# Kernel tuning notes

Measured on AMD Instinct MI355X. Metric: run time of the kernel, lower is better.

The kernel has to match this reference:

```python
import jax, jax.numpy as jnp
import numpy as np

B, M, N = 2097152, 6, 3
SQUARINGS = 8   # fixed scaling: ||T||_F <~ sqrt(M) ~ 2.5, so ||A|| ~ 0.01 after scaling
ORDER = 12     # Taylor order; gives ~machine precision at this scaled norm


def _expm(T):
    """Batched matrix exponential via fixed scaling-and-squaring + Horner Taylor.
    T: [B, N, N]. Numerically matches torch.matrix_exp for these well-scaled inputs."""
    A = T / (2.0 ** SQUARINGS)
    I = jnp.eye(T.shape[-1], dtype=T.dtype)
    # Horner: exp(A) ~ I + A(I + A/2(I + ... (I + A/ORDER)))
    E = I + A / ORDER
    for k in range(ORDER - 1, 0, -1):
        E = I + jnp.matmul(A / k, E)
    for _ in range(SQUARINGS):
        E = jnp.matmul(E, E)
    return E


def setup_inputs() -> dict:
    key = jax.random.key(0)
    kx, kc, kp = jax.random.split(key, 3)
    x = jax.random.normal(kx, (B, N, 1), dtype=jnp.float32)
    c = jax.random.normal(kc, (B, M), dtype=jnp.float32)
    psi = jax.random.normal(kp, (M, N, N), dtype=jnp.float32) * 0.1
    # per-dictionary-element Frobenius normalization, as in __init__
    psi = psi / jnp.linalg.norm(psi.reshape(M, -1), axis=1)[:, None, None]
    return {"x": x, "c": c, "psi": psi}


def reference(x, c, psi):
    # T[b] = sum_m c[b,m] * psi[m]  -> [B, N, N]
    T = jnp.einsum('bm,mij->bij', c, psi)
    return jnp.matmul(_expm(T), x)  # [B, N, 1]
```

## Files before the change

kernel.cpp:

```cpp
#include <hip/hip_runtime.h>

__global__ __launch_bounds__(256) void expm_kernel(
    const float* __restrict__ x,
    const float* __restrict__ c,
    const float* __restrict__ psi,
    float* __restrict__ out,
    int B)
{
    const int b = blockIdx.x * blockDim.x + threadIdx.x;
    if (b >= B) return;

    const float2* c2 = reinterpret_cast<const float2*>(c + (size_t)b * 6);
    const float2 ca = c2[0], cb = c2[1], cc = c2[2];
    const float cm[6] = {ca.x * 0.0625f, ca.y * 0.0625f,
                         cb.x * 0.0625f, cb.y * 0.0625f,
                         cc.x * 0.0625f, cc.y * 0.0625f};

    float A[9];
#pragma unroll
    for (int j = 0; j < 9; ++j) {
        float s = cm[0] * psi[0 * 9 + j];
#pragma unroll
        for (int m = 1; m < 6; ++m) s = fmaf(cm[m], psi[m * 9 + j], s);
        A[j] = s;
    }

    float E[9];
#pragma unroll
    for (int j = 0; j < 9; ++j) E[j] = A[j] * (1.0f / 6.0f);
    E[0] += 1.0f; E[4] += 1.0f; E[8] += 1.0f;

#pragma unroll
    for (int k = 5; k >= 1; --k) {
        const float rk = 1.0f / (float)k;
        float Tm[9];
#pragma unroll
        for (int i = 0; i < 3; ++i) {
#pragma unroll
            for (int j = 0; j < 3; ++j) {
                float s = A[i * 3 + 0] * E[0 * 3 + j];
                s = fmaf(A[i * 3 + 1], E[1 * 3 + j], s);
                s = fmaf(A[i * 3 + 2], E[2 * 3 + j], s);
                Tm[i * 3 + j] = s;
            }
        }
#pragma unroll
        for (int j = 0; j < 9; ++j) E[j] = fmaf(Tm[j], rk, (j == 0 || j == 4 || j == 8) ? 1.0f : 0.0f);
    }

#pragma unroll
    for (int s4 = 0; s4 < 2; ++s4) {
        float Tm[9];
#pragma unroll
        for (int i = 0; i < 3; ++i) {
#pragma unroll
            for (int j = 0; j < 3; ++j) {
                float v = E[i * 3 + 0] * E[0 * 3 + j];
                v = fmaf(E[i * 3 + 1], E[1 * 3 + j], v);
                v = fmaf(E[i * 3 + 2], E[2 * 3 + j], v);
                Tm[i * 3 + j] = v;
            }
        }
#pragma unroll
        for (int j = 0; j < 9; ++j) E[j] = Tm[j];
    }

    const float* xb = x + (size_t)b * 3;
    float y0 = xb[0], y1 = xb[1], y2 = xb[2];
#pragma unroll
    for (int r = 0; r < 4; ++r) {
        const float t0 = fmaf(E[0], y0, fmaf(E[1], y1, E[2] * y2));
        const float t1 = fmaf(E[3], y0, fmaf(E[4], y1, E[5] * y2));
        const float t2 = fmaf(E[6], y0, fmaf(E[7], y1, E[8] * y2));
        y0 = t0; y1 = t1; y2 = t2;
    }

    float* ob = out + (size_t)b * 3;
    ob[0] = y0; ob[1] = y1; ob[2] = y2;
}

extern "C" void kernel_launch(void* const* d_in, const int* in_sizes, int n_in,
                              void* d_out, int out_size, void* d_ws, size_t ws_size,
                              hipStream_t stream) {
    const float* x   = (const float*)d_in[0];
    const float* c   = (const float*)d_in[1];
    const float* psi = (const float*)d_in[2];
    float* out = (float*)d_out;

    const int B = in_sizes[1] / 6;
    const int block = 256;
    const int grid = (B + block - 1) / block;
    expm_kernel<<<grid, block, 0, stream>>>(x, c, psi, out, B);
}
```

Baseline: 108.7 us.

## Replace Taylor Horner chain with Cayley-Hamilton quadratic polynomial for 3x3 expm

Computes the trace, principal-minor sum and determinant of the scaled 3x3 matrix, then runs a scalar recurrence to reduce the order-12 Taylor series to a0*I + a1*A + a2*A^2 via Cayley-Hamilton. This removes five 3x3 matmuls of Horner and two squarings, leaving one A^2 product. The scaling changes from 1/16 to 1/4 with only the final four matrix-vector repetitions left, so accuracy relies on the truncated series at a larger norm and on the numerical stability of the recurrence.

After: 104.8 us. -3.6%, faster.

```diff
diff --git a/kernel.cpp b/kernel.cpp
--- a/kernel.cpp
+++ b/kernel.cpp
@@ -12,9 +12,9 @@
 
     const float2* c2 = reinterpret_cast<const float2*>(c + (size_t)b * 6);
     const float2 ca = c2[0], cb = c2[1], cc = c2[2];
-    const float cm[6] = {ca.x * 0.0625f, ca.y * 0.0625f,
-                         cb.x * 0.0625f, cb.y * 0.0625f,
-                         cc.x * 0.0625f, cc.y * 0.0625f};
+    const float cm[6] = {ca.x * 0.25f, ca.y * 0.25f,
+                         cb.x * 0.25f, cb.y * 0.25f,
+                         cc.x * 0.25f, cc.y * 0.25f};
 
     float A[9];
 #pragma unroll
@@ -25,45 +25,53 @@
         A[j] = s;
     }
 
+    const float tr = A[0] + A[4] + A[8];
+    const float m01 = fmaf(A[0], A[4], -A[1] * A[3]);
+    const float m02 = fmaf(A[0], A[8], -A[2] * A[6]);
+    const float m12 = fmaf(A[4], A[8], -A[5] * A[7]);
+    const float msum = m01 + m02 + m12;
+    const float M10 = fmaf(A[3], A[8], -A[5] * A[6]);
+    const float M20 = fmaf(A[3], A[7], -A[4] * A[6]);
+    const float det = fmaf(A[0], m12, fmaf(-A[1], M10, A[2] * M20));
+    const float c2v = tr, c1v = -msum, c0v = det;
+
+    float p0 = 0.0f, p1 = 0.0f, p2 = 1.0f;
+    float a0 = 1.0f, a1 = 1.0f, a2 = 0.5f;
+    const float invfact[13] = {0, 0, 0,
+        1.6666667e-1f,
+        4.1666667e-2f,
+        8.3333333e-3f,
+        1.3888889e-3f,
+        1.9841270e-4f,
+        2.4801587e-5f,
+        2.7557319e-6f,
+        2.7557319e-7f,
+        2.5052108e-8f,
+        2.0876757e-9f};
+#pragma unroll
+    for (int k = 3; k <= 12; ++k) {
+        const float t0 = c0v * p2;
+        const float t1 = fmaf(c1v, p2, p0);
+        const float t2 = fmaf(c2v, p2, p1);
+        p0 = t0; p1 = t1; p2 = t2;
+        const float f = invfact[k];
+        a0 = fmaf(p0, f, a0);
+        a1 = fmaf(p1, f, a1);
+        a2 = fmaf(p2, f, a2);
+    }
+
     float E[9];
 #pragma unroll
-    for (int j = 0; j < 9; ++j) E[j] = A[j] * (1.0f / 6.0f);
-    E[0] += 1.0f; E[4] += 1.0f; E[8] += 1.0f;
-
+    for (int i = 0; i < 3; ++i) {
 #pragma unroll
-    for (int k = 5; k >= 1; --k) {
-        const float rk = 1.0f / (float)k;
-        float Tm[9];
-#pragma unroll
-        for (int i = 0; i < 3; ++i) {
-#pragma unroll
-            for (int j = 0; j < 3; ++j) {
-                float s = A[i * 3 + 0] * E[0 * 3 + j];
-                s = fmaf(A[i * 3 + 1], E[1 * 3 + j], s);
-                s = fmaf(A[i * 3 + 2], E[2 * 3 + j], s);
-                Tm[i * 3 + j] = s;
-            }
+        for (int j = 0; j < 3; ++j) {
+            float v = A[i * 3 + 0] * A[0 * 3 + j];
+            v = fmaf(A[i * 3 + 1], A[1 * 3 + j], v);
+            v = fmaf(A[i * 3 + 2], A[2 * 3 + j], v);
+            E[i * 3 + j] = fmaf(a2, v, a1 * A[i * 3 + j]);
         }
-#pragma unroll
-        for (int j = 0; j < 9; ++j) E[j] = fmaf(Tm[j], rk, (j == 0 || j == 4 || j == 8) ? 1.0f : 0.0f);
     }
-
-#pragma unroll
-    for (int s4 = 0; s4 < 2; ++s4) {
-        float Tm[9];
-#pragma unroll
-        for (int i = 0; i < 3; ++i) {
-#pragma unroll
-            for (int j = 0; j < 3; ++j) {
-                float v = E[i * 3 + 0] * E[0 * 3 + j];
-                v = fmaf(E[i * 3 + 1], E[1 * 3 + j], v);
-                v = fmaf(E[i * 3 + 2], E[2 * 3 + j], v);
-                Tm[i * 3 + j] = v;
-            }
-        }
-#pragma unroll
-        for (int j = 0; j < 9; ++j) E[j] = Tm[j];
-    }
+    E[0] += a0; E[4] += a0; E[8] += a0;
 
     const float* xb = x + (size_t)b * 3;
     float y0 = xb[0], y1 = xb[1], y2 = xb[2];
```
